# Kernel tuning notes

Hardware: AMD Instinct MI355X
Metric: run time of the kernel (lower is better)

## Reference

```python
import jax, jax.numpy as jnp
import numpy as np

B, F_SIZE, DIM = 2048, 32, 64
LAYER_SIZES = (128, 128)


def setup_inputs() -> dict:
    key = jax.random.key(0)
    k1, k2, k3 = jax.random.split(key, 3)
    inputs = jax.random.normal(k1, (B, F_SIZE, DIM), dtype=jnp.float32)
    # Conv1d(kernel=1) weights: (out_channels, in_channels)
    W0 = jax.random.normal(k2, (128, F_SIZE * F_SIZE), dtype=jnp.float32) * 0.03
    b0 = jnp.zeros((128,), dtype=jnp.float32)
    # split_half -> field_nums[1] = 64 -> in_channels = 64 * 32 = 2048
    W1 = jax.random.normal(k3, (128, 64 * F_SIZE), dtype=jnp.float32) * 0.03
    b1 = jnp.zeros((128,), dtype=jnp.float32)
    return {"inputs": inputs, "W0": W0, "b0": b0, "W1": W1, "b1": b1}


def _cin_forward(inputs, Ws, bs):
    batch, _, dim = inputs.shape
    x0 = inputs
    h = inputs
    finals = []
    n_layers = len(Ws)
    for i in range(n_layers):
        H = h.shape[1]
        M = x0.shape[1]
        # outer-product interaction: (b, H, M, d) -> (b, H*M, d)
        z = jnp.einsum('bhd,bmd->bhmd', h, x0).reshape(batch, H * M, dim)
        # 1x1 conv == per-position channel matmul
        out = jnp.einsum('bcd,oc->bod', z, Ws[i]) + bs[i][None, :, None]
        out = jax.nn.relu(out)
        size = Ws[i].shape[0]
        if i != n_layers - 1:
            # split_half: first half feeds next layer, second half is output
            h = out[:, : size // 2, :]
            finals.append(out[:, size // 2 :, :])
        else:
            finals.append(out)
    result = jnp.concatenate(finals, axis=1)  # (b, 64 + 128, d)
    return jnp.sum(result, axis=-1)           # (b, 192)


def reference(inputs, W0, b0, W1, b1):
    return _cin_forward(inputs, (W0, W1), (b0, b1))
```

## Files before the change

kernel.cpp:

```cpp
#include <hip/hip_runtime.h>
#include <hip/hip_bf16.h>


#define BATCH 2048
#define FSZ   32
#define DIM   64
#define K0    1024
#define K1    2048
#define OUTC  192

#define W0_FRAGS 16384
#define W1_FRAGS 32768
#define W0_ELEMS (128 * K0)

typedef _Float16 v8h __attribute__((ext_vector_type(8)));
typedef float    v4f __attribute__((ext_vector_type(4)));

#define XT_PITCH 40
#define XD_PITCH 66
#define HD_PITCH 66

__global__ void convert_w_kernel(const float* __restrict__ W0,
                                 const float* __restrict__ W1,
                                 _Float16* __restrict__ wsw) {
    int t = blockIdx.x * blockDim.x + threadIdx.x;
    if (t < W0_FRAGS) {
        int ks = t >> 9, s = (t >> 6) & 7, lane = t & 63;
        int row = s * 16 + (lane & 15);
        int k0  = ks * 32 + (lane >> 4) * 8;
        const float* src = W0 + (size_t)row * K0 + k0;
        _Float16* dst = wsw + (size_t)t * 8;
        #pragma unroll
        for (int j = 0; j < 8; ++j) dst[j] = (_Float16)src[j];
    } else if (t < W0_FRAGS + W1_FRAGS) {
        int u = t - W0_FRAGS;
        int ks = u >> 9, s = (u >> 6) & 7, lane = u & 63;
        int row = s * 16 + (lane & 15);
        int k0  = ks * 32 + (lane >> 4) * 8;
        const float* src = W1 + (size_t)row * K1 + k0;
        _Float16* dst = wsw + W0_ELEMS + (size_t)u * 8;
        #pragma unroll
        for (int j = 0; j < 8; ++j) dst[j] = (_Float16)src[j];
    }
}

__global__ __launch_bounds__(256, 4) void cin_kernel(
    const float* __restrict__ X,
    const float* __restrict__ b0,
    const float* __restrict__ b1,
    const _Float16* __restrict__ Wsw,
    float* __restrict__ out)
{
    __shared__ _Float16 xT[DIM * XT_PITCH];
    __shared__ _Float16 xD[FSZ * XD_PITCH];
    __shared__ _Float16 h1D[64 * HD_PITCH];

    const int b    = blockIdx.x;
    const int tid  = threadIdx.x;
    const int wave = tid >> 6;
    const int lane = tid & 63;
    const int quad = lane >> 4;
    const int col  = lane & 15;

    const float* xb = X + (size_t)b * (FSZ * DIM);
    #pragma unroll
    for (int i = tid; i < FSZ * DIM; i += 256) {
        int m = i >> 6, d = i & 63;
        _Float16 v = (_Float16)xb[i];
        xT[d * XT_PITCH + m] = v;
        xD[m * XD_PITCH + d] = v;
    }
    __syncthreads();

    v8h xv8[4];
    int dd[4];
    #pragma unroll
    for (int t = 0; t < 4; ++t) {
        dd[t] = 16 * t + col;
        xv8[t] = *(const v8h*)(&xT[dd[t] * XT_PITCH + quad * 8]);
    }

    v4f acc[2][4];
    #pragma unroll
    for (int r = 0; r < 2; ++r)
        #pragma unroll
        for (int t = 0; t < 4; ++t) acc[r][t] = (v4f)0.0f;

    {
        const _Float16* Wk = Wsw + (size_t)wave * 2 * 512 + (size_t)lane * 8;
        #pragma unroll 4
        for (int ks = 0; ks < 32; ++ks) {
            v8h a0 = *(const v8h*)(Wk);
            v8h a1 = *(const v8h*)(Wk + 512);
            Wk += 4096;
            #pragma unroll
            for (int t = 0; t < 4; ++t) {
                _Float16 s = xD[ks * XD_PITCH + dd[t]];
                v8h s8 = {s, s, s, s, s, s, s, s};
                v8h bfr = s8 * xv8[t];
                acc[0][t] = __builtin_amdgcn_mfma_f32_16x16x32_f16(a0, bfr, acc[0][t], 0, 0, 0);
                acc[1][t] = __builtin_amdgcn_mfma_f32_16x16x32_f16(a1, bfr, acc[1][t], 0, 0, 0);
            }
        }
    }

    #pragma unroll
    for (int r = 0; r < 2; ++r) {
        const int obase = wave * 32 + r * 16 + quad * 4;
        if (obase < 64) {
            #pragma unroll
            for (int reg = 0; reg < 4; ++reg) {
                float bias = b0[obase + reg];
                #pragma unroll
                for (int t = 0; t < 4; ++t) {
                    float v = acc[r][t][reg] + bias;
                    v = v > 0.0f ? v : 0.0f;
                    h1D[(obase + reg) * HD_PITCH + dd[t]] = (_Float16)v;
                }
            }
        } else {
            #pragma unroll
            for (int reg = 0; reg < 4; ++reg) {
                float bias = b0[obase + reg];
                float s = 0.0f;
                #pragma unroll
                for (int t = 0; t < 4; ++t) {
                    float v = acc[r][t][reg] + bias;
                    s += (v > 0.0f ? v : 0.0f);
                }
                s += __shfl_xor(s, 1);
                s += __shfl_xor(s, 2);
                s += __shfl_xor(s, 4);
                s += __shfl_xor(s, 8);
                if (col == 0) out[(size_t)b * OUTC + (obase + reg - 64)] = s;
            }
        }
    }
    __syncthreads();

    #pragma unroll
    for (int r = 0; r < 2; ++r)
        #pragma unroll
        for (int t = 0; t < 4; ++t) acc[r][t] = (v4f)0.0f;

    {
        const _Float16* Wk = Wsw + W0_ELEMS + (size_t)wave * 2 * 512 + (size_t)lane * 8;
        #pragma unroll 4
        for (int ks = 0; ks < 64; ++ks) {
            v8h a0 = *(const v8h*)(Wk);
            v8h a1 = *(const v8h*)(Wk + 512);
            Wk += 4096;
            #pragma unroll
            for (int t = 0; t < 4; ++t) {
                _Float16 s = h1D[ks * HD_PITCH + dd[t]];
                v8h s8 = {s, s, s, s, s, s, s, s};
                v8h bfr = s8 * xv8[t];
                acc[0][t] = __builtin_amdgcn_mfma_f32_16x16x32_f16(a0, bfr, acc[0][t], 0, 0, 0);
                acc[1][t] = __builtin_amdgcn_mfma_f32_16x16x32_f16(a1, bfr, acc[1][t], 0, 0, 0);
            }
        }
    }

    #pragma unroll
    for (int r = 0; r < 2; ++r) {
        const int obase = wave * 32 + r * 16 + quad * 4;
        #pragma unroll
        for (int reg = 0; reg < 4; ++reg) {
            float bias = b1[obase + reg];
            float s = 0.0f;
            #pragma unroll
            for (int t = 0; t < 4; ++t) {
                float v = acc[r][t][reg] + bias;
                s += (v > 0.0f ? v : 0.0f);
            }
            s += __shfl_xor(s, 1);
            s += __shfl_xor(s, 2);
            s += __shfl_xor(s, 4);
            s += __shfl_xor(s, 8);
            if (col == 0) out[(size_t)b * OUTC + 64 + obase + reg] = s;
        }
    }
}

extern "C" void kernel_launch(void* const* d_in, const int* in_sizes, int n_in,
                              void* d_out, int out_size, void* d_ws, size_t ws_size,
                              hipStream_t stream) {
    const float* X  = (const float*)d_in[0];
    const float* W0 = (const float*)d_in[1];
    const float* b0 = (const float*)d_in[2];
    const float* W1 = (const float*)d_in[3];
    const float* b1 = (const float*)d_in[4];
    float* out = (float*)d_out;
    _Float16* wsw = (_Float16*)d_ws;

    convert_w_kernel<<<(W0_FRAGS + W1_FRAGS + 255) / 256, 256, 0, stream>>>(W0, W1, wsw);
    cin_kernel<<<BATCH, 256, 0, stream>>>(X, b0, b1, wsw, out);
}
```

Baseline: 161.0 us.

## Switch to 32x32x16 MFMA tiles and process two batch rows per block

Each block now handles two batch elements: two waves per batch element, each wave computing 64 output channels over all 64 positions with 32x32x16 MFMAs. The weight layout is reswizzled to match. Since the four waves share the same weight fragments, each fragment pulled from global or L2 serves two batch rows. Broadcast x and h1 values are stored pre-duplicated as half2 words in LDS and biases are staged there too. LDS use rises and the occupancy hint drops from 4 to 3, and the larger accumulators raise register pressure.

```diff
diff --git a/kernel.cpp b/kernel.cpp
--- a/kernel.cpp
+++ b/kernel.cpp
@@ -1,185 +1,206 @@
 #include <hip/hip_runtime.h>
-#include <hip/hip_bf16.h>
-
-
-#define BATCH 2048
-#define FSZ   32
-#define DIM   64
-#define K0    1024
-#define K1    2048
-#define OUTC  192
-
-#define W0_FRAGS 16384
-#define W1_FRAGS 32768
-#define W0_ELEMS (128 * K0)
-
-typedef _Float16 v8h __attribute__((ext_vector_type(8)));
-typedef float    v4f __attribute__((ext_vector_type(4)));
-
-#define XT_PITCH 40
-#define XD_PITCH 66
-#define HD_PITCH 66
+
+
+#define K0 1024
+#define K1 2048
+#define OUTC 192
+#define L0_ELEMS (128 * K0)
+#define L1_ELEMS (128 * K1)
+#define L0_FRAGS (L0_ELEMS / 8)
+#define L1_FRAGS (L1_ELEMS / 8)
+
+typedef _Float16 v8h  __attribute__((ext_vector_type(8)));
+typedef _Float16 v2h  __attribute__((ext_vector_type(2)));
+typedef float    v16f __attribute__((ext_vector_type(16)));
 
 __global__ void convert_w_kernel(const float* __restrict__ W0,
                                  const float* __restrict__ W1,
                                  _Float16* __restrict__ wsw) {
     int t = blockIdx.x * blockDim.x + threadIdx.x;
-    if (t < W0_FRAGS) {
-        int ks = t >> 9, s = (t >> 6) & 7, lane = t & 63;
-        int row = s * 16 + (lane & 15);
-        int k0  = ks * 32 + (lane >> 4) * 8;
-        const float* src = W0 + (size_t)row * K0 + k0;
-        _Float16* dst = wsw + (size_t)t * 8;
-        #pragma unroll
-        for (int j = 0; j < 8; ++j) dst[j] = (_Float16)src[j];
-    } else if (t < W0_FRAGS + W1_FRAGS) {
-        int u = t - W0_FRAGS;
-        int ks = u >> 9, s = (u >> 6) & 7, lane = u & 63;
-        int row = s * 16 + (lane & 15);
-        int k0  = ks * 32 + (lane >> 4) * 8;
-        const float* src = W1 + (size_t)row * K1 + k0;
-        _Float16* dst = wsw + W0_ELEMS + (size_t)u * 8;
-        #pragma unroll
-        for (int j = 0; j < 8; ++j) dst[j] = (_Float16)src[j];
-    }
-}
-
-__global__ __launch_bounds__(256, 4) void cin_kernel(
+    if (t >= L0_FRAGS + L1_FRAGS) return;
+    const float* src;
+    _Float16* dst;
+    if (t < L0_FRAGS) {
+        int lane = t & 63, rt = (t >> 6) & 3, ks = t >> 8;
+        int row = rt * 32 + (lane & 31);
+        int k   = ks * 16 + (lane >> 5) * 8;
+        src = W0 + (size_t)row * K0 + k;
+        dst = wsw + (size_t)t * 8;
+    } else {
+        int u = t - L0_FRAGS;
+        int lane = u & 63, rt = (u >> 6) & 3, ks = u >> 8;
+        int row = rt * 32 + (lane & 31);
+        int k   = ks * 16 + (lane >> 5) * 8;
+        src = W1 + (size_t)row * K1 + k;
+        dst = wsw + L0_ELEMS + (size_t)u * 8;
+    }
+    #pragma unroll
+    for (int j = 0; j < 8; ++j) dst[j] = (_Float16)src[j];
+}
+
+__device__ __forceinline__ v8h dup8(v2h s) {
+    return __builtin_shufflevector(s, s, 0, 1, 0, 1, 0, 1, 0, 1);
+}
+
+__global__ __launch_bounds__(256, 3) void cin_kernel(
     const float* __restrict__ X,
     const float* __restrict__ b0,
     const float* __restrict__ b1,
     const _Float16* __restrict__ Wsw,
     float* __restrict__ out)
 {
-    __shared__ _Float16 xT[DIM * XT_PITCH];
-    __shared__ _Float16 xD[FSZ * XD_PITCH];
-    __shared__ _Float16 h1D[64 * HD_PITCH];
-
-    const int b    = blockIdx.x;
+    __shared__ uint32_t xDup[2][32 * 64];
+    __shared__ uint32_t h1Dup[2][64 * 64];
+    __shared__ float biasLds[256];
+
     const int tid  = threadIdx.x;
     const int wave = tid >> 6;
     const int lane = tid & 63;
-    const int quad = lane >> 4;
-    const int col  = lane & 15;
-
-    const float* xb = X + (size_t)b * (FSZ * DIM);
-    #pragma unroll
-    for (int i = tid; i < FSZ * DIM; i += 256) {
-        int m = i >> 6, d = i & 63;
-        _Float16 v = (_Float16)xb[i];
-        xT[d * XT_PITCH + m] = v;
-        xD[m * XD_PITCH + d] = v;
+    const int bi   = wave >> 1;
+    const int rw   = wave & 1;
+    const int l31  = lane & 31;
+    const int hi   = lane >> 5;
+    const size_t bb = (size_t)blockIdx.x * 2;
+
+    if (tid < 128) biasLds[tid] = b0[tid];
+    else           biasLds[tid] = b1[tid - 128];
+
+    const float* xsrc = X + bb * 2048;
+    for (int i = tid; i < 4096; i += 256) {
+        int bby = i >> 11, loc = i & 2047;
+        int m = loc >> 6, d = loc & 63;
+        _Float16 h = (_Float16)xsrc[i];
+        _Float16* xT = (_Float16*)&h1Dup[bby][0];
+        xT[d * 40 + m] = h;
+        v2h p = {h, h};
+        xDup[bby][m * 64 + d] = __builtin_bit_cast(uint32_t, p);
     }
     __syncthreads();
 
-    v8h xv8[4];
-    int dd[4];
-    #pragma unroll
-    for (int t = 0; t < 4; ++t) {
-        dd[t] = 16 * t + col;
-        xv8[t] = *(const v8h*)(&xT[dd[t] * XT_PITCH + quad * 8]);
-    }
-
-    v4f acc[2][4];
-    #pragma unroll
-    for (int r = 0; r < 2; ++r)
-        #pragma unroll
-        for (int t = 0; t < 4; ++t) acc[r][t] = (v4f)0.0f;
-
+    v8h xv[2][2];
     {
-        const _Float16* Wk = Wsw + (size_t)wave * 2 * 512 + (size_t)lane * 8;
+        const _Float16* xT = (const _Float16*)&h1Dup[bi][0];
+        #pragma unroll
+        for (int c = 0; c < 2; ++c)
+            #pragma unroll
+            for (int p = 0; p < 2; ++p)
+                xv[c][p] = *(const v8h*)&xT[(c * 32 + l31) * 40 + p * 16 + hi * 8];
+    }
+    __syncthreads();
+
+    v16f acc[2][2];
+    #pragma unroll
+    for (int rt = 0; rt < 2; ++rt)
+        #pragma unroll
+        for (int c = 0; c < 2; ++c) acc[rt][c] = (v16f)0.0f;
+
+    {
+        const _Float16* Wp = Wsw + (size_t)rw * 1024 + (size_t)lane * 8;
         #pragma unroll 4
-        for (int ks = 0; ks < 32; ++ks) {
-            v8h a0 = *(const v8h*)(Wk);
-            v8h a1 = *(const v8h*)(Wk + 512);
-            Wk += 4096;
+        for (int h = 0; h < 32; ++h) {
+            v8h a00 = *(const v8h*)(Wp);
+            v8h a10 = *(const v8h*)(Wp + 512);
+            v8h a01 = *(const v8h*)(Wp + 2048);
+            v8h a11 = *(const v8h*)(Wp + 2560);
+            Wp += 4096;
+            v2h s0 = __builtin_bit_cast(v2h, xDup[bi][h * 64 + l31]);
+            v2h s1 = __builtin_bit_cast(v2h, xDup[bi][h * 64 + 32 + l31]);
+            v8h s80 = dup8(s0), s81 = dup8(s1);
+            v8h b00 = s80 * xv[0][0], b01 = s80 * xv[0][1];
+            v8h b10 = s81 * xv[1][0], b11 = s81 * xv[1][1];
+            acc[0][0] = __builtin_amdgcn_mfma_f32_32x32x16_f16(a00, b00, acc[0][0], 0, 0, 0);
+            acc[1][0] = __builtin_amdgcn_mfma_f32_32x32x16_f16(a10, b00, acc[1][0], 0, 0, 0);
+            acc[0][1] = __builtin_amdgcn_mfma_f32_32x32x16_f16(a00, b10, acc[0][1], 0, 0, 0);
+            acc[1][1] = __builtin_amdgcn_mfma_f32_32x32x16_f16(a10, b10, acc[1][1], 0, 0, 0);
+            acc[0][0] = __builtin_amdgcn_mfma_f32_32x32x16_f16(a01, b01, acc[0][0], 0, 0, 0);
+            acc[1][0] = __builtin_amdgcn_mfma_f32_32x32x16_f16(a11, b01, acc[1][0], 0, 0, 0);
+            acc[0][1] = __builtin_amdgcn_mfma_f32_32x32x16_f16(a01, b11, acc[0][1], 0, 0, 0);
+            acc[1][1] = __builtin_amdgcn_mfma_f32_32x32x16_f16(a11, b11, acc[1][1], 0, 0, 0);
+        }
+    }
+
+    if (rw == 0) {
+        #pragma unroll
+        for (int rt = 0; rt < 2; ++rt)
             #pragma unroll
-            for (int t = 0; t < 4; ++t) {
-                _Float16 s = xD[ks * XD_PITCH + dd[t]];
-                v8h s8 = {s, s, s, s, s, s, s, s};
-                v8h bfr = s8 * xv8[t];
-                acc[0][t] = __builtin_amdgcn_mfma_f32_16x16x32_f16(a0, bfr, acc[0][t], 0, 0, 0);
-                acc[1][t] = __builtin_amdgcn_mfma_f32_16x16x32_f16(a1, bfr, acc[1][t], 0, 0, 0);
-            }
-        }
-    }
-
-    #pragma unroll
-    for (int r = 0; r < 2; ++r) {
-        const int obase = wave * 32 + r * 16 + quad * 4;
-        if (obase < 64) {
-            #pragma unroll
-            for (int reg = 0; reg < 4; ++reg) {
-                float bias = b0[obase + reg];
+            for (int reg = 0; reg < 16; ++reg) {
+                int row = rt * 32 + (reg & 3) + 8 * (reg >> 2) + 4 * hi;
+                float bias = biasLds[row];
                 #pragma unroll
-                for (int t = 0; t < 4; ++t) {
-                    float v = acc[r][t][reg] + bias;
+                for (int c = 0; c < 2; ++c) {
+                    float v = acc[rt][c][reg] + bias;
                     v = v > 0.0f ? v : 0.0f;
-                    h1D[(obase + reg) * HD_PITCH + dd[t]] = (_Float16)v;
+                    _Float16 hv = (_Float16)v;
+                    v2h p = {hv, hv};
+                    h1Dup[bi][row * 64 + c * 32 + l31] = __builtin_bit_cast(uint32_t, p);
                 }
             }
-        } else {
+    } else {
+        #pragma unroll
+        for (int rt = 0; rt < 2; ++rt)
             #pragma unroll
-            for (int reg = 0; reg < 4; ++reg) {
-                float bias = b0[obase + reg];
-                float s = 0.0f;
-                #pragma unroll
-                for (int t = 0; t < 4; ++t) {
-                    float v = acc[r][t][reg] + bias;
-                    s += (v > 0.0f ? v : 0.0f);
-                }
+            for (int reg = 0; reg < 16; ++reg) {
+                int grow = 64 + rt * 32 + (reg & 3) + 8 * (reg >> 2) + 4 * hi;
+                float bias = biasLds[grow];
+                float v0 = acc[rt][0][reg] + bias;
+                float v1 = acc[rt][1][reg] + bias;
+                float s = (v0 > 0.0f ? v0 : 0.0f) + (v1 > 0.0f ? v1 : 0.0f);
                 s += __shfl_xor(s, 1);
                 s += __shfl_xor(s, 2);
                 s += __shfl_xor(s, 4);
                 s += __shfl_xor(s, 8);
-                if (col == 0) out[(size_t)b * OUTC + (obase + reg - 64)] = s;
+                s += __shfl_xor(s, 16);
+                if (l31 == 0) out[(bb + bi) * OUTC + (grow - 64)] = s;
             }
+    }
+    __syncthreads();
+
+    #pragma unroll
+    for (int rt = 0; rt < 2; ++rt)
+        #pragma unroll
+        for (int c = 0; c < 2; ++c) acc[rt][c] = (v16f)0.0f;
+
+    {
+        const _Float16* Wp = Wsw + L0_ELEMS + (size_t)rw * 1024 + (size_t)lane * 8;
+        #pragma unroll 4
+        for (int h = 0; h < 64; ++h) {
+            v8h a00 = *(const v8h*)(Wp);
+            v8h a10 = *(const v8h*)(Wp + 512);
+            v8h a01 = *(const v8h*)(Wp + 2048);
+            v8h a11 = *(const v8h*)(Wp + 2560);
+            Wp += 4096;
+            v2h s0 = __builtin_bit_cast(v2h, h1Dup[bi][h * 64 + l31]);
+            v2h s1 = __builtin_bit_cast(v2h, h1Dup[bi][h * 64 + 32 + l31]);
+            v8h s80 = dup8(s0), s81 = dup8(s1);
+            v8h b00 = s80 * xv[0][0], b01 = s80 * xv[0][1];
+            v8h b10 = s81 * xv[1][0], b11 = s81 * xv[1][1];
+            acc[0][0] = __builtin_amdgcn_mfma_f32_32x32x16_f16(a00, b00, acc[0][0], 0, 0, 0);
+            acc[1][0] = __builtin_amdgcn_mfma_f32_32x32x16_f16(a10, b00, acc[1][0], 0, 0, 0);
+            acc[0][1] = __builtin_amdgcn_mfma_f32_32x32x16_f16(a00, b10, acc[0][1], 0, 0, 0);
+            acc[1][1] = __builtin_amdgcn_mfma_f32_32x32x16_f16(a10, b10, acc[1][1], 0, 0, 0);
+            acc[0][0] = __builtin_amdgcn_mfma_f32_32x32x16_f16(a01, b01, acc[0][0], 0, 0, 0);
+            acc[1][0] = __builtin_amdgcn_mfma_f32_32x32x16_f16(a11, b01, acc[1][0], 0, 0, 0);
+            acc[0][1] = __builtin_amdgcn_mfma_f32_32x32x16_f16(a01, b11, acc[0][1], 0, 0, 0);
+            acc[1][1] = __builtin_amdgcn_mfma_f32_32x32x16_f16(a11, b11, acc[1][1], 0, 0, 0);
         }
     }
-    __syncthreads();
-
-    #pragma unroll
-    for (int r = 0; r < 2; ++r)
-        #pragma unroll
-        for (int t = 0; t < 4; ++t) acc[r][t] = (v4f)0.0f;
-
-    {
-        const _Float16* Wk = Wsw + W0_ELEMS + (size_t)wave * 2 * 512 + (size_t)lane * 8;
-        #pragma unroll 4
-        for (int ks = 0; ks < 64; ++ks) {
-            v8h a0 = *(const v8h*)(Wk);
-            v8h a1 = *(const v8h*)(Wk + 512);
-            Wk += 4096;
-            #pragma unroll
-            for (int t = 0; t < 4; ++t) {
-                _Float16 s = h1D[ks * HD_PITCH + dd[t]];
-                v8h s8 = {s, s, s, s, s, s, s, s};
-                v8h bfr = s8 * xv8[t];
-                acc[0][t] = __builtin_amdgcn_mfma_f32_16x16x32_f16(a0, bfr, acc[0][t], 0, 0, 0);
-                acc[1][t] = __builtin_amdgcn_mfma_f32_16x16x32_f16(a1, bfr, acc[1][t], 0, 0, 0);
-            }
-        }
-    }
-
-    #pragma unroll
-    for (int r = 0; r < 2; ++r) {
-        const int obase = wave * 32 + r * 16 + quad * 4;
-        #pragma unroll
-        for (int reg = 0; reg < 4; ++reg) {
-            float bias = b1[obase + reg];
-            float s = 0.0f;
-            #pragma unroll
-            for (int t = 0; t < 4; ++t) {
-                float v = acc[r][t][reg] + bias;
-                s += (v > 0.0f ? v : 0.0f);
-            }
+
+    #pragma unroll
+    for (int rt = 0; rt < 2; ++rt)
+        #pragma unroll
+        for (int reg = 0; reg < 16; ++reg) {
+            int grow = rw * 64 + rt * 32 + (reg & 3) + 8 * (reg >> 2) + 4 * hi;
+            float bias = biasLds[128 + grow];
+            float v0 = acc[rt][0][reg] + bias;
+            float v1 = acc[rt][1][reg] + bias;
+            float s = (v0 > 0.0f ? v0 : 0.0f) + (v1 > 0.0f ? v1 : 0.0f);
             s += __shfl_xor(s, 1);
             s += __shfl_xor(s, 2);
             s += __shfl_xor(s, 4);
             s += __shfl_xor(s, 8);
-            if (col == 0) out[(size_t)b * OUTC + 64 + obase + reg] = s;
+            s += __shfl_xor(s, 16);
+            if (l31 == 0) out[(bb + bi) * OUTC + 64 + grow] = s;
         }
-    }
 }
 
 extern "C" void kernel_launch(void* const* d_in, const int* in_sizes, int n_in,
@@ -193,6 +214,6 @@
     float* out = (float*)d_out;
     _Float16* wsw = (_Float16*)d_ws;
 
-    convert_w_kernel<<<(W0_FRAGS + W1_FRAGS + 255) / 256, 256, 0, stream>>>(W0, W1, wsw);
-    cin_kernel<<<BATCH, 256, 0, stream>>>(X, b0, b1, wsw, out);
-}
+    convert_w_kernel<<<(L0_FRAGS + L1_FRAGS + 255) / 256, 256, 0, stream>>>(W0, W1, wsw);
+    cin_kernel<<<1024, 256, 0, stream>>>(X, b0, b1, wsw, out);
+}
```

Result: slower. 181.3 us (+12.6%).
